# Kernel tuning notes

Measured on AMD Instinct MI355X. Metric: run time of the kernel, lower is better.

Reference implementation:

```python
import jax, jax.numpy as jnp
import numpy as np

N_NODES = 50000
N_EDGES = 800000
D_IN = 128
D_OUT = 128
N_GRAPHS = 64
NEG_SLOPE = 0.01  # torch F.leaky_relu default


def gcn_conv(x, W, b, src, dst, n_nodes):
    """PyG GCNConv: linear, add self-loops, symmetric norm, scatter-add, bias."""
    h = x @ W  # [N, D_OUT]
    # degree including self-loop (edge_weight = 1)
    deg = jnp.zeros((n_nodes,), x.dtype).at[dst].add(1.0) + 1.0
    dinv = jax.lax.rsqrt(deg)
    norm = dinv[src] * dinv[dst]           # [E]
    agg = jnp.zeros_like(h).at[dst].add(h[src] * norm[:, None])
    # self-loop contribution: dinv[i]*dinv[i]*h[i] = h[i]/deg[i]
    return agg + h * (1.0 / deg)[:, None] + b


def gcn_branch(x, edge_index, Ws, bs):
    src, dst = edge_index[0], edge_index[1]
    n = x.shape[0]
    for W, b in zip(Ws, bs):
        x = gcn_conv(x, W, b, src, dst, n)
        x = jax.nn.leaky_relu(x, NEG_SLOPE)
        # dropout is identity in eval mode
    return x


def mean_pool(x, batch, num_graphs):
    s = jax.ops.segment_sum(x, batch, num_segments=num_graphs)
    cnt = jax.ops.segment_sum(jnp.ones((x.shape[0],), x.dtype), batch, num_segments=num_graphs)
    return s / jnp.maximum(cnt, 1.0)[:, None]


def setup_inputs() -> dict:
    key = jax.random.key(0)
    ks = jax.random.split(key, 20)
    inp = {
        'x1': jax.random.normal(ks[0], (N_NODES, D_IN), jnp.float32),
        'edge_index1': jax.random.randint(ks[1], (2, N_EDGES), 0, N_NODES, jnp.int64 if jax.config.jax_enable_x64 else jnp.int32),
        'batch1': jnp.sort(jax.random.randint(ks[2], (N_NODES,), 0, N_GRAPHS)),
        'x2': jax.random.normal(ks[3], (N_NODES, D_IN), jnp.float32),
        'edge_index2': jax.random.randint(ks[4], (2, N_EDGES), 0, N_NODES, jnp.int64 if jax.config.jax_enable_x64 else jnp.int32),
        'batch2': jnp.sort(jax.random.randint(ks[5], (N_NODES,), 0, N_GRAPHS)),
    }
    s = 1.0 / np.sqrt(D_IN)
    inp['W1_0'] = jax.random.uniform(ks[6], (D_IN, D_OUT), jnp.float32, -s, s)
    inp['b1_0'] = jnp.zeros((D_OUT,), jnp.float32)
    inp['W1_1'] = jax.random.uniform(ks[7], (D_OUT, D_OUT), jnp.float32, -s, s)
    inp['b1_1'] = jnp.zeros((D_OUT,), jnp.float32)
    inp['W2_0'] = jax.random.uniform(ks[8], (D_IN, D_OUT), jnp.float32, -s, s)
    inp['b2_0'] = jnp.zeros((D_OUT,), jnp.float32)
    inp['W2_1'] = jax.random.uniform(ks[9], (D_OUT, D_OUT), jnp.float32, -s, s)
    inp['b2_1'] = jnp.zeros((D_OUT,), jnp.float32)
    s2 = 1.0 / np.sqrt(2 * D_OUT)
    inp['lin1_W'] = jax.random.uniform(ks[10], (2 * D_OUT, D_OUT), jnp.float32, -s2, s2)
    inp['lin1_b'] = jax.random.uniform(ks[11], (D_OUT,), jnp.float32, -s2, s2)
    s3 = 1.0 / np.sqrt(D_OUT)
    inp['lin2_W'] = jax.random.uniform(ks[12], (D_OUT, 1), jnp.float32, -s3, s3)
    inp['lin2_b'] = jax.random.uniform(ks[13], (1,), jnp.float32, -s3, s3)
    return inp


def reference(x1, edge_index1, batch1, x2, edge_index2, batch2,
              W1_0, b1_0, W1_1, b1_1, W2_0, b2_0, W2_1, b2_1,
              lin1_W, lin1_b, lin2_W, lin2_b):
    h1 = gcn_branch(x1, edge_index1, [W1_0, W1_1], [b1_0, b1_1])
    h1 = mean_pool(h1, batch1, N_GRAPHS)
    h2 = gcn_branch(x2, edge_index2, [W2_0, W2_1], [b2_0, b2_1])
    h2 = mean_pool(h2, batch2, N_GRAPHS)
    h = jnp.concatenate([h1, h2], axis=-1)  # [G, 256]
    h = jax.nn.relu(h @ lin1_W + lin1_b)
    return h @ lin2_W + lin2_b  # [G, 1]
```

## Files before the change

### kernel.cpp

```cpp
#include <hip/hip_runtime.h>
#include <hip/hip_fp16.h>

#define N_NODES 50000
#define N_EDGES 800000
#define D 128
#define N_GRAPHS 64
#define NEG_SLOPE 0.01f
#define ELLW 32
#define OVF_CAP 8192

#define BUCKETS 196
#define NPAD (BUCKETS * 256)
#define EPB 4096
#define BCAP 5120
#define XS 136

typedef _Float16 half8 __attribute__((ext_vector_type(8)));
typedef _Float16 half4 __attribute__((ext_vector_type(4)));
typedef float f32x4 __attribute__((ext_vector_type(4)));
typedef float f32x2 __attribute__((ext_vector_type(2)));

__device__ __forceinline__ int lower_bound_i(const int* __restrict__ arr, int n, int key) {
    int lo = 0, hi = n;
    while (lo < hi) {
        int mid = (lo + hi) >> 1;
        if (arr[mid] < key) lo = mid + 1; else hi = mid;
    }
    return lo;
}

__global__ __launch_bounds__(256) void k_prep(const float* __restrict__ Wa, const float* __restrict__ Wb,
                                              const float* __restrict__ Wc, const float* __restrict__ Wd,
                                              const int* __restrict__ batch1, const int* __restrict__ batch2,
                                              __half* __restrict__ WtH, int* __restrict__ gcnt,
                                              float* __restrict__ pp, int* __restrict__ cntg) {
    const float* Ws[4] = {Wa, Wb, Wc, Wd};
    const float* W = Ws[blockIdx.x];
    __half* o = WtH + (size_t)blockIdx.x * 16384;
    int t = threadIdx.x;
    for (int r = 0; r < 64; r++) {
        int e = r * 256 + t;
        int k = e >> 7, n = e & 127;
        o[n * 128 + k] = __float2half(W[k * 128 + n]);
    }
#pragma unroll
    for (int i = 0; i < 16; i++) pp[blockIdx.x * 4096 + i * 256 + t] = 0.0f;
    if (blockIdx.x == 0) {
        for (int i = t; i < 2 * BUCKETS + 8; i += 256) gcnt[i] = 0;
    }
    if (blockIdx.x == 1) {
        if (t < 64)
            cntg[t] = lower_bound_i(batch1, N_NODES, t + 1) - lower_bound_i(batch1, N_NODES, t);
        else if (t < 128)
            cntg[t] = lower_bound_i(batch2, N_NODES, (t - 64) + 1) - lower_bound_i(batch2, N_NODES, t - 64);
    }
}

__global__ __launch_bounds__(256) void k_part(const int* __restrict__ ei1, const int* __restrict__ ei2,
                                              int* __restrict__ gcnt, int2* __restrict__ bucketed) {
    const int br = blockIdx.y;
    const int* __restrict__ src = (br ? ei2 : ei1);
    const int* __restrict__ dst = src + N_EDGES;
    int* __restrict__ gc = gcnt + br * BUCKETS;
    int2* __restrict__ bk = bucketed + (size_t)br * BUCKETS * BCAP;

    __shared__ int bcnt[BUCKETS];
    __shared__ int bofs[BUCKETS];
    __shared__ int gbase[BUCKETS];
    __shared__ int sc[BUCKETS];
    __shared__ int stot;
    __shared__ int2 stage[EPB];
    const int tid = threadIdx.x;
    const int base = blockIdx.x * EPB;
    for (int b = tid; b < BUCKETS; b += 256) bcnt[b] = 0;
    __syncthreads();
    int d_[16], s_[16], p_[16];
#pragma unroll
    for (int k = 0; k < 16; k++) {
        int i = base + k * 256 + tid;
        bool v = i < N_EDGES;
        d_[k] = v ? dst[i] : -1;
        s_[k] = v ? src[i] : 0;
        p_[k] = 0;
        if (v) p_[k] = atomicAdd(&bcnt[d_[k] >> 8], 1);
    }
    __syncthreads();
    if (tid < BUCKETS) sc[tid] = bcnt[tid];
    __syncthreads();
    for (int off = 1; off < BUCKETS; off <<= 1) {
        int v = (tid < BUCKETS && tid >= off) ? sc[tid - off] : 0;
        __syncthreads();
        if (tid < BUCKETS) sc[tid] += v;
        __syncthreads();
    }
    if (tid < BUCKETS) {
        bofs[tid] = sc[tid] - bcnt[tid];
        gbase[tid] = atomicAdd(&gc[tid], bcnt[tid]);
    }
    if (tid == BUCKETS - 1) stot = sc[tid];
    __syncthreads();
#pragma unroll
    for (int k = 0; k < 16; k++) {
        if (d_[k] >= 0) stage[bofs[d_[k] >> 8] + p_[k]] = make_int2(d_[k], s_[k]);
    }
    __syncthreads();
    int total = stot;
    for (int i = tid; i < total; i += 256) {
        int2 e = stage[i];
        int b = e.x >> 8;
        int dest = gbase[b] + (i - bofs[b]);
        if (dest < BCAP) bk[(size_t)b * BCAP + dest] = e;
    }
}

__global__ __launch_bounds__(256) void k_build(const int* __restrict__ gcnt, const int2* __restrict__ bucketed,
                                               int* __restrict__ cnti, unsigned short* __restrict__ ell,
                                               int2* __restrict__ ovf, int* __restrict__ ocnt) {
    const int br = blockIdx.y;
    const int* __restrict__ gc = gcnt + br * BUCKETS;
    const int2* __restrict__ bk = bucketed + (size_t)br * BUCKETS * BCAP;
    int* __restrict__ ci = cnti + br * NPAD;
    unsigned short* __restrict__ el = ell + (size_t)br * NPAD * ELLW;
    int2* __restrict__ ov = ovf + (size_t)br * OVF_CAP;
    int* __restrict__ oc = ocnt + br;

    __shared__ unsigned short lell[256 * ELLW];
    __shared__ int lcnt[256];
    const int b = blockIdx.x, tid = threadIdx.x;
    lcnt[tid] = 0;
    __syncthreads();
    int nb = min(gc[b], BCAP);
    const int2* __restrict__ bp = bk + (size_t)b * BCAP;
    for (int i = tid; i < nb; i += 256) {
        int2 e = bp[i];
        int dl = e.x & 255;
        int p = atomicAdd(&lcnt[dl], 1);
        if (p < ELLW) {
            lell[dl * ELLW + p] = (unsigned short)e.y;
        } else {
            int o = atomicAdd(oc, 1);
            if (o < OVF_CAP) ov[o] = e;
        }
    }
    __syncthreads();
    ci[b * 256 + tid] = lcnt[tid];
    uint4* eg = (uint4*)(el + (size_t)b * 256 * ELLW);
    const uint4* elc = (const uint4*)lell;
    for (int i = tid; i < 256 * ELLW * 2 / 16; i += 256) eg[i] = elc[i];
}

__global__ __launch_bounds__(256) void k_gemm(const float* __restrict__ x1, const float* __restrict__ x2,
                                              const __half* __restrict__ WtHall,
                                              const int* __restrict__ cnti, unsigned char* __restrict__ H8) {
    const int br = blockIdx.y;
    const float* __restrict__ x = (br ? x2 : x1);
    const __half* __restrict__ WtH = WtHall + (size_t)(br * 2 + 0) * 16384;
    const int* __restrict__ cnt = cnti + br * NPAD;
    unsigned char* __restrict__ h = H8 + (size_t)br * N_NODES * 128;

    __shared__ _Float16 Xl[64 * XS];
    __shared__ _Float16 Wt[128 * XS];
    const int tid = threadIdx.x;
    const int w = tid >> 6, lane = tid & 63;
    const int quad = lane >> 4, l16 = lane & 15;
    const int row0 = blockIdx.x * 64;

#pragma unroll
    for (int i = 0; i < 8; i++) {
        int i2 = tid + 256 * i;
        int r = i2 >> 4, cg = i2 & 15;
        *(uint4*)&Wt[r * XS + cg * 8] = ((const uint4*)WtH)[i2];
    }
#pragma unroll
    for (int i = 0; i < 8; i++) {
        int i2 = tid + 256 * i;
        int r = i2 >> 5, f4 = i2 & 31;
        float4 v = make_float4(0.f, 0.f, 0.f, 0.f);
        if (row0 + r < N_NODES) v = *(const float4*)(x + (size_t)(row0 + r) * D + f4 * 4);
        half4 hv;
        hv[0] = (_Float16)v.x; hv[1] = (_Float16)v.y; hv[2] = (_Float16)v.z; hv[3] = (_Float16)v.w;
        *(half4*)&Xl[r * XS + f4 * 4] = hv;
    }
    __syncthreads();

    half8 a[4];
#pragma unroll
    for (int kb = 0; kb < 4; kb++)
        a[kb] = *(const half8*)&Xl[(w * 16 + l16) * XS + kb * 32 + quad * 8];

    const int rbase = row0 + w * 16 + quad * 4;
    float di[4];
#pragma unroll
    for (int reg = 0; reg < 4; reg++) {
        int r = rbase + reg;
        di[reg] = (r < N_NODES) ? rsqrtf((float)cnt[r] + 1.0f) : 0.0f;
    }

    float accs[8][4];
#pragma unroll
    for (int ct = 0; ct < 8; ct++) {
        f32x4 acc = {0.f, 0.f, 0.f, 0.f};
#pragma unroll
        for (int kb = 0; kb < 4; kb++) {
            half8 b = *(const half8*)&Wt[(ct * 16 + l16) * XS + kb * 32 + quad * 8];
            acc = __builtin_amdgcn_mfma_f32_16x16x32_f16(a[kb], b, acc, 0, 0, 0);
        }
#pragma unroll
        for (int reg = 0; reg < 4; reg++) accs[ct][reg] = acc[reg] * di[reg];
    }

    __syncthreads();
    unsigned char* S = (unsigned char*)Xl;
#pragma unroll
    for (int ct = 0; ct < 8; ct++)
#pragma unroll
        for (int reg = 0; reg < 4; reg++) {
            int p = __builtin_amdgcn_cvt_pk_fp8_f32(accs[ct][reg], accs[ct][reg], 0, false);
            S[(w * 16 + quad * 4 + reg) * 128 + ct * 16 + l16] = (unsigned char)p;
        }
    __syncthreads();
#pragma unroll
    for (int i = 0; i < 2; i++) {
        int idx = tid + 256 * i;
        int r = idx >> 3, cg = idx & 7;
        if (row0 + r < N_NODES)
            ((uint4*)(h + (size_t)(row0 + r) * 128))[cg] = ((const uint4*)S)[idx];
    }
}

__global__ __launch_bounds__(256) void k_aggemm(const int* __restrict__ cnti, const unsigned short* __restrict__ ell,
                                                const int2* __restrict__ ovf, const int* __restrict__ ocnt,
                                                const unsigned char* __restrict__ H8in,
                                                const float* __restrict__ bias1, const float* __restrict__ bias2,
                                                const __half* __restrict__ WtHall,
                                                unsigned char* __restrict__ H8out) {
    const int br = blockIdx.y;
    const int* __restrict__ cnt = cnti + br * NPAD;
    const unsigned short* __restrict__ el = ell + (size_t)br * NPAD * ELLW;
    const int2* __restrict__ ov = ovf + (size_t)br * OVF_CAP;
    const unsigned char* __restrict__ H8 = H8in + (size_t)br * N_NODES * 128;
    const float* __restrict__ bias = (br ? bias2 : bias1);
    const __half* __restrict__ WtH = WtHall + (size_t)(br * 2 + 1) * 16384;
    unsigned char* __restrict__ hout = H8out + (size_t)br * N_NODES * 128;

    __shared__ _Float16 Xl[64 * XS];
    __shared__ _Float16 Wt[128 * XS];
    const int tid = threadIdx.x;
    const int w = tid >> 6, lane = tid & 63;
    const int quad = lane >> 4, l16 = lane & 15;
    const int l32 = tid & 31;
    const int hw = tid >> 5;
    const int row0 = blockIdx.x * 64;

#pragma unroll
    for (int i = 0; i < 8; i++) {
        int i2 = tid + 256 * i;
        int r = i2 >> 4, cg = i2 & 15;
        *(uint4*)&Wt[r * XS + cg * 8] = ((const uint4*)WtH)[i2];
    }

    float4 bv = ((const float4*)bias)[l32];
    for (int t = 0; t < 8; t++) {
        const int r = hw * 8 + t;
        const int node = row0 + r;
        const bool valid = node < N_NODES;
        int n = valid ? cnt[node] : 0;
        int nc = min(n, ELLW);
        int sv = 0;
        if (l32 < nc) sv = (int)el[(size_t)node * ELLW + l32];

        float4 acc[8];
        if (valid) {
            unsigned int dw = *(const unsigned int*)(H8 + (size_t)node * 128 + l32 * 4);
            f32x2 lo = __builtin_amdgcn_cvt_pk_f32_fp8((int)dw, false);
            f32x2 hi = __builtin_amdgcn_cvt_pk_f32_fp8((int)dw, true);
            acc[0] = make_float4(lo[0], lo[1], hi[0], hi[1]);
        } else {
            acc[0] = make_float4(0.f, 0.f, 0.f, 0.f);
        }
#pragma unroll
        for (int i = 1; i < 8; i++) acc[i] = make_float4(0.f, 0.f, 0.f, 0.f);

        for (int j = 0; j < nc; j += 8) {
            int s[8]; float wt[8];
#pragma unroll
            for (int i = 0; i < 8; i++) {
                s[i] = __shfl(sv, j + i, 32);
                wt[i] = ((j + i) < nc) ? 1.0f : 0.0f;
            }
#pragma unroll
            for (int i = 0; i < 8; i++) {
                unsigned int dw = *(const unsigned int*)(H8 + (size_t)s[i] * 128 + l32 * 4);
                f32x2 lo = __builtin_amdgcn_cvt_pk_f32_fp8((int)dw, false);
                f32x2 hi = __builtin_amdgcn_cvt_pk_f32_fp8((int)dw, true);
                acc[i].x = fmaf(wt[i], lo[0], acc[i].x);
                acc[i].y = fmaf(wt[i], lo[1], acc[i].y);
                acc[i].z = fmaf(wt[i], hi[0], acc[i].z);
                acc[i].w = fmaf(wt[i], hi[1], acc[i].w);
            }
        }
        if (n > ELLW) {
            int oc = min(ocnt[br], OVF_CAP);
            for (int o = 0; o < oc; o++) {
                int2 p = ov[o];
                if (p.x == node) {
                    unsigned int dw = *(const unsigned int*)(H8 + (size_t)p.y * 128 + l32 * 4);
                    f32x2 lo = __builtin_amdgcn_cvt_pk_f32_fp8((int)dw, false);
                    f32x2 hi = __builtin_amdgcn_cvt_pk_f32_fp8((int)dw, true);
                    acc[0].x += lo[0]; acc[0].y += lo[1]; acc[0].z += hi[0]; acc[0].w += hi[1];
                }
            }
        }
        float sx = ((acc[0].x + acc[1].x) + (acc[2].x + acc[3].x)) + ((acc[4].x + acc[5].x) + (acc[6].x + acc[7].x));
        float sy = ((acc[0].y + acc[1].y) + (acc[2].y + acc[3].y)) + ((acc[4].y + acc[5].y) + (acc[6].y + acc[7].y));
        float sz = ((acc[0].z + acc[1].z) + (acc[2].z + acc[3].z)) + ((acc[4].z + acc[5].z) + (acc[6].z + acc[7].z));
        float sw = ((acc[0].w + acc[1].w) + (acc[2].w + acc[3].w)) + ((acc[4].w + acc[5].w) + (acc[6].w + acc[7].w));
        float dv = rsqrtf((float)n + 1.0f);
        float vx = sx * dv + bv.x;
        float vy = sy * dv + bv.y;
        float vz = sz * dv + bv.z;
        float vw = sw * dv + bv.w;
        vx = vx > 0.0f ? vx : NEG_SLOPE * vx;
        vy = vy > 0.0f ? vy : NEG_SLOPE * vy;
        vz = vz > 0.0f ? vz : NEG_SLOPE * vz;
        vw = vw > 0.0f ? vw : NEG_SLOPE * vw;
        union { __half2 h2[2]; uint2 u; } up;
        if (valid) {
            up.h2[0] = __floats2half2_rn(vx, vy);
            up.h2[1] = __floats2half2_rn(vz, vw);
        } else {
            up.u = make_uint2(0u, 0u);
        }
        *(uint2*)&Xl[r * XS + l32 * 4] = up.u;
    }
    __syncthreads();

    half8 a[4];
#pragma unroll
    for (int kb = 0; kb < 4; kb++)
        a[kb] = *(const half8*)&Xl[(w * 16 + l16) * XS + kb * 32 + quad * 8];

    const int rbase = row0 + w * 16 + quad * 4;
    float di[4];
#pragma unroll
    for (int reg = 0; reg < 4; reg++) {
        int r = rbase + reg;
        di[reg] = (r < N_NODES) ? rsqrtf((float)cnt[r] + 1.0f) : 0.0f;
    }

    float accs[8][4];
#pragma unroll
    for (int ct = 0; ct < 8; ct++) {
        f32x4 acc = {0.f, 0.f, 0.f, 0.f};
#pragma unroll
        for (int kb = 0; kb < 4; kb++) {
            half8 b = *(const half8*)&Wt[(ct * 16 + l16) * XS + kb * 32 + quad * 8];
            acc = __builtin_amdgcn_mfma_f32_16x16x32_f16(a[kb], b, acc, 0, 0, 0);
        }
#pragma unroll
        for (int reg = 0; reg < 4; reg++) accs[ct][reg] = acc[reg] * di[reg];
    }

    __syncthreads();
    unsigned char* S = (unsigned char*)Xl;
#pragma unroll
    for (int ct = 0; ct < 8; ct++)
#pragma unroll
        for (int reg = 0; reg < 4; reg++) {
            int p = __builtin_amdgcn_cvt_pk_fp8_f32(accs[ct][reg], accs[ct][reg], 0, false);
            S[(w * 16 + quad * 4 + reg) * 128 + ct * 16 + l16] = (unsigned char)p;
        }
    __syncthreads();
#pragma unroll
    for (int i = 0; i < 2; i++) {
        int idx = tid + 256 * i;
        int r = idx >> 3, cg = idx & 7;
        if (row0 + r < N_NODES)
            ((uint4*)(hout + (size_t)(row0 + r) * 128))[cg] = ((const uint4*)S)[idx];
    }
}

__global__ __launch_bounds__(256) void k_aggpool(const int* __restrict__ cnti, const unsigned short* __restrict__ ell,
                                                 const int2* __restrict__ ovf, const int* __restrict__ ocnt,
                                                 const unsigned char* __restrict__ H8all,
                                                 const float* __restrict__ bias1, const float* __restrict__ bias2,
                                                 const int* __restrict__ batch1, const int* __restrict__ batch2,
                                                 float* __restrict__ ppall) {
    const int br = blockIdx.y;
    const int* __restrict__ cnt = cnti + br * NPAD;
    const unsigned short* __restrict__ el = ell + (size_t)br * NPAD * ELLW;
    const int2* __restrict__ ov = ovf + (size_t)br * OVF_CAP;
    const unsigned char* __restrict__ H8 = H8all + (size_t)br * N_NODES * 128;
    const float* __restrict__ bias = (br ? bias2 : bias1);
    const int* __restrict__ batch = (br ? batch2 : batch1);
    float* __restrict__ pp = ppall + (size_t)br * N_GRAPHS * D;

    const int tid = threadIdx.x;
    const int l32 = tid & 31;
    const int hw = tid >> 5;
    const int node = blockIdx.x * 8 + hw;
    int n = cnt[node];
    int nc = min(n, ELLW);
    int sv = 0;
    if (l32 < nc) sv = (int)el[(size_t)node * ELLW + l32];
    int ncOther = __shfl(nc, (tid & 63) ^ 32, 64);
    int jmax = max(nc, ncOther);

    float4 acc[8];
    {
        unsigned int dw = *(const unsigned int*)(H8 + (size_t)node * 128 + l32 * 4);
        f32x2 lo = __builtin_amdgcn_cvt_pk_f32_fp8((int)dw, false);
        f32x2 hi = __builtin_amdgcn_cvt_pk_f32_fp8((int)dw, true);
        acc[0] = make_float4(lo[0], lo[1], hi[0], hi[1]);
    }
#pragma unroll
    for (int i = 1; i < 8; i++) acc[i] = make_float4(0.f, 0.f, 0.f, 0.f);

    for (int j = 0; j < jmax; j += 8) {
        int s[8]; float wt[8];
#pragma unroll
        for (int i = 0; i < 8; i++) {
            s[i] = __shfl(sv, j + i, 32);
            wt[i] = ((j + i) < nc) ? 1.0f : 0.0f;
        }
#pragma unroll
        for (int i = 0; i < 8; i++) {
            unsigned int dw = *(const unsigned int*)(H8 + (size_t)s[i] * 128 + l32 * 4);
            f32x2 lo = __builtin_amdgcn_cvt_pk_f32_fp8((int)dw, false);
            f32x2 hi = __builtin_amdgcn_cvt_pk_f32_fp8((int)dw, true);
            acc[i].x = fmaf(wt[i], lo[0], acc[i].x);
            acc[i].y = fmaf(wt[i], lo[1], acc[i].y);
            acc[i].z = fmaf(wt[i], hi[0], acc[i].z);
            acc[i].w = fmaf(wt[i], hi[1], acc[i].w);
        }
    }
    if (n > ELLW) {
        int oc = min(ocnt[br], OVF_CAP);
        for (int o = 0; o < oc; o++) {
            int2 p = ov[o];
            if (p.x == node) {
                unsigned int dw = *(const unsigned int*)(H8 + (size_t)p.y * 128 + l32 * 4);
                f32x2 lo = __builtin_amdgcn_cvt_pk_f32_fp8((int)dw, false);
                f32x2 hi = __builtin_amdgcn_cvt_pk_f32_fp8((int)dw, true);
                acc[0].x += lo[0]; acc[0].y += lo[1]; acc[0].z += hi[0]; acc[0].w += hi[1];
            }
        }
    }
    float sx = ((acc[0].x + acc[1].x) + (acc[2].x + acc[3].x)) + ((acc[4].x + acc[5].x) + (acc[6].x + acc[7].x));
    float sy = ((acc[0].y + acc[1].y) + (acc[2].y + acc[3].y)) + ((acc[4].y + acc[5].y) + (acc[6].y + acc[7].y));
    float sz = ((acc[0].z + acc[1].z) + (acc[2].z + acc[3].z)) + ((acc[4].z + acc[5].z) + (acc[6].z + acc[7].z));
    float sw = ((acc[0].w + acc[1].w) + (acc[2].w + acc[3].w)) + ((acc[4].w + acc[5].w) + (acc[6].w + acc[7].w));
    float dv = rsqrtf((float)n + 1.0f);
    float4 b = ((const float4*)bias)[l32];
    float vx = sx * dv + b.x;
    float vy = sy * dv + b.y;
    float vz = sz * dv + b.z;
    float vw = sw * dv + b.w;
    vx = vx > 0.0f ? vx : NEG_SLOPE * vx;
    vy = vy > 0.0f ? vy : NEG_SLOPE * vy;
    vz = vz > 0.0f ? vz : NEG_SLOPE * vz;
    vw = vw > 0.0f ? vw : NEG_SLOPE * vw;
    __half2 q0 = __floats2half2_rn(vx, vy);
    __half2 q1 = __floats2half2_rn(vz, vw);
    float2 f0 = __half22float2(q0);
    float2 f1 = __half22float2(q1);

    __shared__ float sacc[8][128];
    __shared__ int sg[8];
    *(float4*)&sacc[hw][l32 * 4] = make_float4(f0.x, f0.y, f1.x, f1.y);
    if (l32 == 0) sg[hw] = batch[node];
    __syncthreads();
    if (tid < 128) {
        float s = sacc[0][tid];
        int g = sg[0];
        for (int r2 = 1; r2 < 8; r2++) {
            if (sg[r2] == g) {
                s += sacc[r2][tid];
            } else {
                atomicAdd(&pp[(size_t)g * D + tid], s);
                s = sacc[r2][tid];
                g = sg[r2];
            }
        }
        atomicAdd(&pp[(size_t)g * D + tid], s);
    }
}

__global__ __launch_bounds__(128) void k_mlp(const float* __restrict__ pp, const int* __restrict__ cntg,
                                             const float* __restrict__ lin1W, const float* __restrict__ lin1b,
                                             const float* __restrict__ lin2W, const float* __restrict__ lin2b,
                                             float* __restrict__ out) {
    int g = blockIdx.x;
    int c = threadIdx.x;
    __shared__ float cat[2 * D];
    cat[c] = pp[(size_t)g * D + c] / fmaxf((float)cntg[g], 1.0f);
    cat[c + D] = pp[(size_t)(N_GRAPHS + g) * D + c] / fmaxf((float)cntg[64 + g], 1.0f);
    __syncthreads();
    float acc = lin1b[c];
#pragma unroll 8
    for (int k = 0; k < 2 * D; k++) acc += cat[k] * lin1W[k * D + c];
    acc = fmaxf(acc, 0.0f);
    float v = acc * lin2W[c];
#pragma unroll
    for (int off = 32; off > 0; off >>= 1) v += __shfl_down(v, off, 64);
    __shared__ float wsum[2];
    if ((c & 63) == 0) wsum[c >> 6] = v;
    __syncthreads();
    if (c == 0) out[g] = wsum[0] + wsum[1] + lin2b[0];
}

extern "C" void kernel_launch(void* const* d_in, const int* in_sizes, int n_in,
                              void* d_out, int out_size, void* d_ws, size_t ws_size,
                              hipStream_t stream) {
    const float* x1 = (const float*)d_in[0];
    const int*   ei1 = (const int*)d_in[1];
    const int*   batch1 = (const int*)d_in[2];
    const float* x2 = (const float*)d_in[3];
    const int*   ei2 = (const int*)d_in[4];
    const int*   batch2 = (const int*)d_in[5];
    const float* W1_0 = (const float*)d_in[6];
    const float* b1_0 = (const float*)d_in[7];
    const float* W1_1 = (const float*)d_in[8];
    const float* b1_1 = (const float*)d_in[9];
    const float* W2_0 = (const float*)d_in[10];
    const float* b2_0 = (const float*)d_in[11];
    const float* W2_1 = (const float*)d_in[12];
    const float* b2_1 = (const float*)d_in[13];
    const float* lin1W = (const float*)d_in[14];
    const float* lin1b = (const float*)d_in[15];
    const float* lin2W = (const float*)d_in[16];
    const float* lin2b = (const float*)d_in[17];
    float* out = (float*)d_out;

    __half* WtH = (__half*)d_ws;
    unsigned char* H8a = (unsigned char*)(WtH + 65536);
    unsigned char* H8b = H8a + 2 * (size_t)N_NODES * 128;
    unsigned short* ell = (unsigned short*)(H8b + 2 * (size_t)N_NODES * 128);
    int2*   bucketed = (int2*)(ell + 2 * (size_t)NPAD * ELLW);
    int*    cnti = (int*)(bucketed + 2 * (size_t)BUCKETS * BCAP);
    int*    gcnt = cnti + 2 * NPAD;
    int*    ocnt = gcnt + 2 * BUCKETS;
    int*    cntg = ocnt + 8;
    int2*   ovf  = (int2*)(cntg + 128);
    float*  pp   = (float*)(ovf + 2 * (size_t)OVF_CAP);

    dim3 b256(256);
    int partBlocks = (N_EDGES + EPB - 1) / EPB;
    int gemmBlocks = (N_NODES + 63) / 64;
    int aggBlocks  = N_NODES / 8;

    k_prep<<<4, b256, 0, stream>>>(W1_0, W1_1, W2_0, W2_1, batch1, batch2, WtH, gcnt, pp, cntg);

    k_part  <<<dim3(partBlocks, 2), b256, 0, stream>>>(ei1, ei2, gcnt, bucketed);
    k_build <<<dim3(BUCKETS, 2),    b256, 0, stream>>>(gcnt, bucketed, cnti, ell, ovf, ocnt);

    k_gemm   <<<dim3(gemmBlocks, 2), b256, 0, stream>>>(x1, x2, WtH, cnti, H8a);
    k_aggemm <<<dim3(gemmBlocks, 2), b256, 0, stream>>>(cnti, ell, ovf, ocnt, H8a, b1_0, b2_0, WtH, H8b);
    k_aggpool<<<dim3(aggBlocks, 2),  b256, 0, stream>>>(cnti, ell, ovf, ocnt, H8b, b1_1, b2_1, batch1, batch2, pp);

    k_mlp<<<N_GRAPHS, dim3(128), 0, stream>>>(pp, cntg, lin1W, lin1b, lin2W, lin2b, out);
}
```

Before: 312.0 us.

## Split fused aggregate+GEMM kernel into separate aggregation and fp16-input GEMM kernels

Replaces the fused layer-1 aggregation+GEMM kernel with a standalone aggregation kernel that writes fp16 activations to a new workspace buffer. A templated GEMM kernel then reads those fp16 activations for the second layer. The point is to give the gather-heavy aggregation more parallelism: 8 nodes per block and no large weight tile in shared memory, so occupancy should rise. The cost is one extra launch and an fp16 activation round trip through global memory.

```diff
diff --git a/kernel.cpp b/kernel.cpp
--- a/kernel.cpp
+++ b/kernel.cpp
@@ -149,12 +149,13 @@
     for (int i = tid; i < 256 * ELLW * 2 / 16; i += 256) eg[i] = elc[i];
 }
 
-__global__ __launch_bounds__(256) void k_gemm(const float* __restrict__ x1, const float* __restrict__ x2,
-                                              const __half* __restrict__ WtHall,
+template <bool FP16IN>
+__global__ __launch_bounds__(256) void k_gemm(const void* __restrict__ xin1, const void* __restrict__ xin2,
+                                              const __half* __restrict__ WtHall, int layer,
                                               const int* __restrict__ cnti, unsigned char* __restrict__ H8) {
     const int br = blockIdx.y;
-    const float* __restrict__ x = (br ? x2 : x1);
-    const __half* __restrict__ WtH = WtHall + (size_t)(br * 2 + 0) * 16384;
+    const void* __restrict__ xin = (br ? xin2 : xin1);
+    const __half* __restrict__ WtH = WtHall + (size_t)(br * 2 + layer) * 16384;
     const int* __restrict__ cnt = cnti + br * NPAD;
     unsigned char* __restrict__ h = H8 + (size_t)br * N_NODES * 128;
 
@@ -171,15 +172,28 @@
         int r = i2 >> 4, cg = i2 & 15;
         *(uint4*)&Wt[r * XS + cg * 8] = ((const uint4*)WtH)[i2];
     }
-#pragma unroll
-    for (int i = 0; i < 8; i++) {
-        int i2 = tid + 256 * i;
-        int r = i2 >> 5, f4 = i2 & 31;
-        float4 v = make_float4(0.f, 0.f, 0.f, 0.f);
-        if (row0 + r < N_NODES) v = *(const float4*)(x + (size_t)(row0 + r) * D + f4 * 4);
-        half4 hv;
-        hv[0] = (_Float16)v.x; hv[1] = (_Float16)v.y; hv[2] = (_Float16)v.z; hv[3] = (_Float16)v.w;
-        *(half4*)&Xl[r * XS + f4 * 4] = hv;
+    if (FP16IN) {
+        const __half* x = (const __half*)xin;
+#pragma unroll
+        for (int i = 0; i < 4; i++) {
+            int i2 = tid + 256 * i;
+            int r = i2 >> 4, cg = i2 & 15;
+            uint4 v = make_uint4(0, 0, 0, 0);
+            if (row0 + r < N_NODES) v = ((const uint4*)(x + (size_t)(row0 + r) * D))[cg];
+            *(uint4*)&Xl[r * XS + cg * 8] = v;
+        }
+    } else {
+        const float* x = (const float*)xin;
+#pragma unroll
+        for (int i = 0; i < 8; i++) {
+            int i2 = tid + 256 * i;
+            int r = i2 >> 5, f4 = i2 & 31;
+            float4 v = make_float4(0.f, 0.f, 0.f, 0.f);
+            if (row0 + r < N_NODES) v = *(const float4*)((const float*)x + (size_t)(row0 + r) * D + f4 * 4);
+            half4 hv;
+            hv[0] = (_Float16)v.x; hv[1] = (_Float16)v.y; hv[2] = (_Float16)v.z; hv[3] = (_Float16)v.w;
+            *(half4*)&Xl[r * XS + f4 * 4] = hv;
+        }
     }
     __syncthreads();
 
@@ -228,156 +242,86 @@
     }
 }
 
-__global__ __launch_bounds__(256) void k_aggemm(const int* __restrict__ cnti, const unsigned short* __restrict__ ell,
-                                                const int2* __restrict__ ovf, const int* __restrict__ ocnt,
-                                                const unsigned char* __restrict__ H8in,
-                                                const float* __restrict__ bias1, const float* __restrict__ bias2,
-                                                const __half* __restrict__ WtHall,
-                                                unsigned char* __restrict__ H8out) {
+__global__ __launch_bounds__(256) void k_agg(const int* __restrict__ cnti, const unsigned short* __restrict__ ell,
+                                             const int2* __restrict__ ovf, const int* __restrict__ ocnt,
+                                             const unsigned char* __restrict__ H8all, const float* __restrict__ bias1,
+                                             const float* __restrict__ bias2, __half* __restrict__ ACT) {
     const int br = blockIdx.y;
     const int* __restrict__ cnt = cnti + br * NPAD;
     const unsigned short* __restrict__ el = ell + (size_t)br * NPAD * ELLW;
     const int2* __restrict__ ov = ovf + (size_t)br * OVF_CAP;
-    const unsigned char* __restrict__ H8 = H8in + (size_t)br * N_NODES * 128;
+    const unsigned char* __restrict__ H8 = H8all + (size_t)br * N_NODES * 128;
     const float* __restrict__ bias = (br ? bias2 : bias1);
-    const __half* __restrict__ WtH = WtHall + (size_t)(br * 2 + 1) * 16384;
-    unsigned char* __restrict__ hout = H8out + (size_t)br * N_NODES * 128;
-
-    __shared__ _Float16 Xl[64 * XS];
-    __shared__ _Float16 Wt[128 * XS];
+    __half* __restrict__ out = ACT + (size_t)br * N_NODES * D;
+
     const int tid = threadIdx.x;
-    const int w = tid >> 6, lane = tid & 63;
-    const int quad = lane >> 4, l16 = lane & 15;
     const int l32 = tid & 31;
-    const int hw = tid >> 5;
-    const int row0 = blockIdx.x * 64;
-
-#pragma unroll
-    for (int i = 0; i < 8; i++) {
-        int i2 = tid + 256 * i;
-        int r = i2 >> 4, cg = i2 & 15;
-        *(uint4*)&Wt[r * XS + cg * 8] = ((const uint4*)WtH)[i2];
-    }
-
-    float4 bv = ((const float4*)bias)[l32];
-    for (int t = 0; t < 8; t++) {
-        const int r = hw * 8 + t;
-        const int node = row0 + r;
-        const bool valid = node < N_NODES;
-        int n = valid ? cnt[node] : 0;
-        int nc = min(n, ELLW);
-        int sv = 0;
-        if (l32 < nc) sv = (int)el[(size_t)node * ELLW + l32];
-
-        float4 acc[8];
-        if (valid) {
-            unsigned int dw = *(const unsigned int*)(H8 + (size_t)node * 128 + l32 * 4);
+    const int node = blockIdx.x * 8 + (tid >> 5);
+    int n = cnt[node];
+    int nc = min(n, ELLW);
+    int sv = 0;
+    if (l32 < nc) sv = (int)el[(size_t)node * ELLW + l32];
+    int ncOther = __shfl(nc, (tid & 63) ^ 32, 64);
+    int jmax = max(nc, ncOther);
+
+    float4 acc[8];
+    {
+        unsigned int dw = *(const unsigned int*)(H8 + (size_t)node * 128 + l32 * 4);
+        f32x2 lo = __builtin_amdgcn_cvt_pk_f32_fp8((int)dw, false);
+        f32x2 hi = __builtin_amdgcn_cvt_pk_f32_fp8((int)dw, true);
+        acc[0] = make_float4(lo[0], lo[1], hi[0], hi[1]);
+    }
+#pragma unroll
+    for (int i = 1; i < 8; i++) acc[i] = make_float4(0.f, 0.f, 0.f, 0.f);
+
+    for (int j = 0; j < jmax; j += 8) {
+        int s[8]; float w[8];
+#pragma unroll
+        for (int i = 0; i < 8; i++) {
+            s[i] = __shfl(sv, j + i, 32);
+            w[i] = ((j + i) < nc) ? 1.0f : 0.0f;
+        }
+#pragma unroll
+        for (int i = 0; i < 8; i++) {
+            unsigned int dw = *(const unsigned int*)(H8 + (size_t)s[i] * 128 + l32 * 4);
             f32x2 lo = __builtin_amdgcn_cvt_pk_f32_fp8((int)dw, false);
             f32x2 hi = __builtin_amdgcn_cvt_pk_f32_fp8((int)dw, true);
-            acc[0] = make_float4(lo[0], lo[1], hi[0], hi[1]);
-        } else {
-            acc[0] = make_float4(0.f, 0.f, 0.f, 0.f);
-        }
-#pragma unroll
-        for (int i = 1; i < 8; i++) acc[i] = make_float4(0.f, 0.f, 0.f, 0.f);
-
-        for (int j = 0; j < nc; j += 8) {
-            int s[8]; float wt[8];
-#pragma unroll
-            for (int i = 0; i < 8; i++) {
-                s[i] = __shfl(sv, j + i, 32);
-                wt[i] = ((j + i) < nc) ? 1.0f : 0.0f;
-            }
-#pragma unroll
-            for (int i = 0; i < 8; i++) {
-                unsigned int dw = *(const unsigned int*)(H8 + (size_t)s[i] * 128 + l32 * 4);
+            acc[i].x = fmaf(w[i], lo[0], acc[i].x);
+            acc[i].y = fmaf(w[i], lo[1], acc[i].y);
+            acc[i].z = fmaf(w[i], hi[0], acc[i].z);
+            acc[i].w = fmaf(w[i], hi[1], acc[i].w);
+        }
+    }
+    if (n > ELLW) {
+        int oc = min(ocnt[br], OVF_CAP);
+        for (int o = 0; o < oc; o++) {
+            int2 p = ov[o];
+            if (p.x == node) {
+                unsigned int dw = *(const unsigned int*)(H8 + (size_t)p.y * 128 + l32 * 4);
                 f32x2 lo = __builtin_amdgcn_cvt_pk_f32_fp8((int)dw, false);
                 f32x2 hi = __builtin_amdgcn_cvt_pk_f32_fp8((int)dw, true);
-                acc[i].x = fmaf(wt[i], lo[0], acc[i].x);
-                acc[i].y = fmaf(wt[i], lo[1], acc[i].y);
-                acc[i].z = fmaf(wt[i], hi[0], acc[i].z);
-                acc[i].w = fmaf(wt[i], hi[1], acc[i].w);
+                acc[0].x += lo[0]; acc[0].y += lo[1]; acc[0].z += hi[0]; acc[0].w += hi[1];
             }
         }
-        if (n > ELLW) {
-            int oc = min(ocnt[br], OVF_CAP);
-            for (int o = 0; o < oc; o++) {
-                int2 p = ov[o];
-                if (p.x == node) {
-                    unsigned int dw = *(const unsigned int*)(H8 + (size_t)p.y * 128 + l32 * 4);
-                    f32x2 lo = __builtin_amdgcn_cvt_pk_f32_fp8((int)dw, false);
-                    f32x2 hi = __builtin_amdgcn_cvt_pk_f32_fp8((int)dw, true);
-                    acc[0].x += lo[0]; acc[0].y += lo[1]; acc[0].z += hi[0]; acc[0].w += hi[1];
-                }
-            }
-        }
-        float sx = ((acc[0].x + acc[1].x) + (acc[2].x + acc[3].x)) + ((acc[4].x + acc[5].x) + (acc[6].x + acc[7].x));
-        float sy = ((acc[0].y + acc[1].y) + (acc[2].y + acc[3].y)) + ((acc[4].y + acc[5].y) + (acc[6].y + acc[7].y));
-        float sz = ((acc[0].z + acc[1].z) + (acc[2].z + acc[3].z)) + ((acc[4].z + acc[5].z) + (acc[6].z + acc[7].z));
-        float sw = ((acc[0].w + acc[1].w) + (acc[2].w + acc[3].w)) + ((acc[4].w + acc[5].w) + (acc[6].w + acc[7].w));
-        float dv = rsqrtf((float)n + 1.0f);
-        float vx = sx * dv + bv.x;
-        float vy = sy * dv + bv.y;
-        float vz = sz * dv + bv.z;
-        float vw = sw * dv + bv.w;
-        vx = vx > 0.0f ? vx : NEG_SLOPE * vx;
-        vy = vy > 0.0f ? vy : NEG_SLOPE * vy;
-        vz = vz > 0.0f ? vz : NEG_SLOPE * vz;
-        vw = vw > 0.0f ? vw : NEG_SLOPE * vw;
-        union { __half2 h2[2]; uint2 u; } up;
-        if (valid) {
-            up.h2[0] = __floats2half2_rn(vx, vy);
-            up.h2[1] = __floats2half2_rn(vz, vw);
-        } else {
-            up.u = make_uint2(0u, 0u);
-        }
-        *(uint2*)&Xl[r * XS + l32 * 4] = up.u;
-    }
-    __syncthreads();
-
-    half8 a[4];
-#pragma unroll
-    for (int kb = 0; kb < 4; kb++)
-        a[kb] = *(const half8*)&Xl[(w * 16 + l16) * XS + kb * 32 + quad * 8];
-
-    const int rbase = row0 + w * 16 + quad * 4;
-    float di[4];
-#pragma unroll
-    for (int reg = 0; reg < 4; reg++) {
-        int r = rbase + reg;
-        di[reg] = (r < N_NODES) ? rsqrtf((float)cnt[r] + 1.0f) : 0.0f;
-    }
-
-    float accs[8][4];
-#pragma unroll
-    for (int ct = 0; ct < 8; ct++) {
-        f32x4 acc = {0.f, 0.f, 0.f, 0.f};
-#pragma unroll
-        for (int kb = 0; kb < 4; kb++) {
-            half8 b = *(const half8*)&Wt[(ct * 16 + l16) * XS + kb * 32 + quad * 8];
-            acc = __builtin_amdgcn_mfma_f32_16x16x32_f16(a[kb], b, acc, 0, 0, 0);
-        }
-#pragma unroll
-        for (int reg = 0; reg < 4; reg++) accs[ct][reg] = acc[reg] * di[reg];
-    }
-
-    __syncthreads();
-    unsigned char* S = (unsigned char*)Xl;
-#pragma unroll
-    for (int ct = 0; ct < 8; ct++)
-#pragma unroll
-        for (int reg = 0; reg < 4; reg++) {
-            int p = __builtin_amdgcn_cvt_pk_fp8_f32(accs[ct][reg], accs[ct][reg], 0, false);
-            S[(w * 16 + quad * 4 + reg) * 128 + ct * 16 + l16] = (unsigned char)p;
-        }
-    __syncthreads();
-#pragma unroll
-    for (int i = 0; i < 2; i++) {
-        int idx = tid + 256 * i;
-        int r = idx >> 3, cg = idx & 7;
-        if (row0 + r < N_NODES)
-            ((uint4*)(hout + (size_t)(row0 + r) * 128))[cg] = ((const uint4*)S)[idx];
-    }
+    }
+    float sx = ((acc[0].x + acc[1].x) + (acc[2].x + acc[3].x)) + ((acc[4].x + acc[5].x) + (acc[6].x + acc[7].x));
+    float sy = ((acc[0].y + acc[1].y) + (acc[2].y + acc[3].y)) + ((acc[4].y + acc[5].y) + (acc[6].y + acc[7].y));
+    float sz = ((acc[0].z + acc[1].z) + (acc[2].z + acc[3].z)) + ((acc[4].z + acc[5].z) + (acc[6].z + acc[7].z));
+    float sw = ((acc[0].w + acc[1].w) + (acc[2].w + acc[3].w)) + ((acc[4].w + acc[5].w) + (acc[6].w + acc[7].w));
+    float dv = rsqrtf((float)n + 1.0f);
+    float4 b = ((const float4*)bias)[l32];
+    float vx = sx * dv + b.x;
+    float vy = sy * dv + b.y;
+    float vz = sz * dv + b.z;
+    float vw = sw * dv + b.w;
+    vx = vx > 0.0f ? vx : NEG_SLOPE * vx;
+    vy = vy > 0.0f ? vy : NEG_SLOPE * vy;
+    vz = vz > 0.0f ? vz : NEG_SLOPE * vz;
+    vw = vw > 0.0f ? vw : NEG_SLOPE * vw;
+    union { __half2 h2[2]; uint2 u; } up;
+    up.h2[0] = __floats2half2_rn(vx, vy);
+    up.h2[1] = __floats2half2_rn(vz, vw);
+    *(uint2*)(out + (size_t)node * 128 + l32 * 4) = up.u;
 }
 
 __global__ __launch_bounds__(256) void k_aggpool(const int* __restrict__ cnti, const unsigned short* __restrict__ ell,
@@ -533,7 +477,8 @@
     float* out = (float*)d_out;
 
     __half* WtH = (__half*)d_ws;
-    unsigned char* H8a = (unsigned char*)(WtH + 65536);
+    __half* ACT = WtH + 65536;
+    unsigned char* H8a = (unsigned char*)(ACT + 2 * (size_t)N_NODES * D);
     unsigned char* H8b = H8a + 2 * (size_t)N_NODES * 128;
     unsigned short* ell = (unsigned short*)(H8b + 2 * (size_t)N_NODES * 128);
     int2*   bucketed = (int2*)(ell + 2 * (size_t)NPAD * ELLW);
@@ -554,9 +499,10 @@
     k_part  <<<dim3(partBlocks, 2), b256, 0, stream>>>(ei1, ei2, gcnt, bucketed);
     k_build <<<dim3(BUCKETS, 2),    b256, 0, stream>>>(gcnt, bucketed, cnti, ell, ovf, ocnt);
 
-    k_gemm   <<<dim3(gemmBlocks, 2), b256, 0, stream>>>(x1, x2, WtH, cnti, H8a);
-    k_aggemm <<<dim3(gemmBlocks, 2), b256, 0, stream>>>(cnti, ell, ovf, ocnt, H8a, b1_0, b2_0, WtH, H8b);
-    k_aggpool<<<dim3(aggBlocks, 2),  b256, 0, stream>>>(cnti, ell, ovf, ocnt, H8b, b1_1, b2_1, batch1, batch2, pp);
+    k_gemm<false><<<dim3(gemmBlocks, 2), b256, 0, stream>>>(x1, x2, WtH, 0, cnti, H8a);
+    k_agg        <<<dim3(aggBlocks, 2),  b256, 0, stream>>>(cnti, ell, ovf, ocnt, H8a, b1_0, b2_0, ACT);
+    k_gemm<true> <<<dim3(gemmBlocks, 2), b256, 0, stream>>>(ACT, ACT + (size_t)N_NODES * D, WtH, 1, cnti, H8b);
+    k_aggpool    <<<dim3(aggBlocks, 2),  b256, 0, stream>>>(cnti, ell, ovf, ocnt, H8b, b1_1, b2_1, batch1, batch2, pp);
 
     k_mlp<<<N_GRAPHS, dim3(128), 0, stream>>>(pp, cntg, lin1W, lin1b, lin2W, lin2b, out);
 }
```

New measurement: 288.6 us. -7.5%, faster.
